# Kernel tuning notes

Hardware: AMD Instinct MI355X
Metric: run time of the kernel (lower is better)

Reference implementation:

```python
import jax, jax.numpy as jnp
import numpy as np

EMBED_DIM = 768
MAX_LEN = 1024
ALPHA = 0.99
BATCH = 16


def setup_inputs() -> dict:
    key = jax.random.key(0)
    k1, k2, k3 = jax.random.split(key, 3)
    x = jax.random.normal(k1, (BATCH, MAX_LEN, EMBED_DIM), dtype=jnp.float32)
    # torch nn.Linear(embed_dim, 3*embed_dim): store weight as [in, out] for x @ W
    scale = 1.0 / np.sqrt(EMBED_DIM)
    W_qkv = jax.random.uniform(k2, (EMBED_DIM, 3 * EMBED_DIM), dtype=jnp.float32,
                               minval=-scale, maxval=scale)
    b_qkv = jax.random.uniform(k3, (3 * EMBED_DIM,), dtype=jnp.float32,
                               minval=-scale, maxval=scale)
    return {"x": x, "W_qkv": W_qkv, "b_qkv": b_qkv}


def _retention_mask(sl, alpha, dtype):
    # M[i, j] = alpha**(i - j) if i >= j else 0 (causal tril * decay)
    i = jnp.arange(sl)[:, None]
    j = jnp.arange(sl)[None, :]
    causal = i >= j
    # compute decay only where causal to avoid huge alpha**(negative) values
    exponent = jnp.where(causal, (i - j).astype(dtype), 0.0)
    decay = jnp.asarray(alpha, dtype) ** exponent
    return jnp.where(causal, decay, jnp.zeros((), dtype))


def reference(x, W_qkv, b_qkv):
    bs, sl, d = x.shape
    qkv = x @ W_qkv + b_qkv                      # [B, S, 3D]
    q, k, v = jnp.split(qkv, 3, axis=-1)         # each [B, S, D]
    M = _retention_mask(sl, ALPHA, x.dtype)      # [S, S]
    scores = jnp.einsum('bsd,btd->bst', q, k) / jnp.sqrt(jnp.asarray(d, x.dtype))
    out = jnp.einsum('bst,btd->bsd', scores * M[None, :, :], v)
    return out
```

## Files before the change

### kernel.cpp

```cpp
#include <hip/hip_runtime.h>
#include <hip/hip_bf16.h>


#define SEQ   1024
#define DIM   768
#define ND3   2304

typedef __attribute__((ext_vector_type(8))) short bf16x8;
typedef __attribute__((ext_vector_type(4))) float f32x4;

#define L2A     (-0.014499569695115089f)
#define RSQRTD  (0.03608439182435161f)

__device__ __forceinline__ unsigned short f2bf(float x) {
  union { float f; unsigned u; } v; v.f = x;
  unsigned r = v.u + 0x7FFFu + ((v.u >> 16) & 1u);
  return (unsigned short)(r >> 16);
}

__device__ __forceinline__ void gload16(const void* g, void* l) {
  __builtin_amdgcn_global_load_lds(
      (const __attribute__((address_space(1))) void*)g,
      (__attribute__((address_space(3))) void*)l, 16, 0, 0);
}

__device__ __forceinline__ void gemm_core(
    const unsigned short* gA, const unsigned short* gA2,
    const unsigned short* gB, const unsigned short* gB2,
    char* lsA, char* lsB, int nt, int wid, int lane, f32x4 acc[2][4]) {
  int lr = lane & 15, lg = lane >> 4;
  int wm = wid >> 1, wn = wid & 1;
  int rdA = (wm * 32 + lr) * 128 + ((lg ^ (lr & 7)) << 4);
  int rdB = (wn * 64 + lr) * 128 + ((lg ^ (lr & 7)) << 4);
  int wo = wid * 2048;

#define STAGE(t, par) do {                                                    \
    int lo_ = ((par) << 14) + wo;                                             \
    gload16(gA  + (size_t)(t) * 64, lsA + lo_);                               \
    gload16(gA2 + (size_t)(t) * 64, lsA + lo_ + 1024);                        \
    gload16(gB  + (size_t)(t) * 64, lsB + lo_);                               \
    gload16(gB2 + (size_t)(t) * 64, lsB + lo_ + 1024);                        \
  } while (0)

  STAGE(0, 0);
  STAGE(1, 1);
  asm volatile("s_waitcnt vmcnt(4)" ::: "memory");
  __builtin_amdgcn_s_barrier();
  asm volatile("" ::: "memory");

  for (int t = 0; t < nt; ++t) {
    int pbase = (t & 1) << 14;
    bf16x8 aF[2][2], bF[2][4];
#pragma unroll
    for (int kh = 0; kh < 2; ++kh) {
#pragma unroll
      for (int f = 0; f < 2; ++f)
        aF[kh][f] = *(const bf16x8*)(lsA + pbase + ((rdA + f * 2048) ^ (kh << 6)));
#pragma unroll
      for (int n = 0; n < 4; ++n)
        bF[kh][n] = *(const bf16x8*)(lsB + pbase + ((rdB + n * 2048) ^ (kh << 6)));
    }
    __builtin_amdgcn_s_setprio(1);
#pragma unroll
    for (int kh = 0; kh < 2; ++kh)
#pragma unroll
      for (int f = 0; f < 2; ++f)
#pragma unroll
        for (int n = 0; n < 4; ++n)
          acc[f][n] = __builtin_amdgcn_mfma_f32_16x16x32_bf16(aF[kh][f], bF[kh][n], acc[f][n], 0, 0, 0);
    __builtin_amdgcn_s_setprio(0);

    if (t == nt - 1) break;
    __builtin_amdgcn_s_barrier();
    asm volatile("" ::: "memory");
    if (t + 2 < nt) {
      STAGE(t + 2, t & 1);
      asm volatile("s_waitcnt vmcnt(4)" ::: "memory");
    } else {
      asm volatile("s_waitcnt vmcnt(0)" ::: "memory");
    }
    __builtin_amdgcn_s_barrier();
    asm volatile("" ::: "memory");
  }
#undef STAGE
}

__global__ void convert_x(const float* __restrict__ x, unsigned short* __restrict__ xb) {
  size_t i = ((size_t)blockIdx.x * 256 + threadIdx.x) * 8;
  float4 f0 = *(const float4*)(x + i);
  float4 f1 = *(const float4*)(x + i + 4);
  bf16x8 v;
  v[0] = (short)f2bf(f0.x); v[1] = (short)f2bf(f0.y);
  v[2] = (short)f2bf(f0.z); v[3] = (short)f2bf(f0.w);
  v[4] = (short)f2bf(f1.x); v[5] = (short)f2bf(f1.y);
  v[6] = (short)f2bf(f1.z); v[7] = (short)f2bf(f1.w);
  *(bf16x8*)(xb + i) = v;
}

__global__ void transpose_w(const float* __restrict__ W, unsigned short* __restrict__ Wt) {
  __shared__ float tile[64][65];
  int n0 = (blockIdx.x % 36) * 64;
  int k0 = (blockIdx.x / 36) * 64;
  int tx = threadIdx.x & 63, ty = threadIdx.x >> 6;
#pragma unroll
  for (int p = 0; p < 16; ++p) {
    int k = ty + p * 4;
    tile[k][tx] = W[(size_t)(k0 + k) * ND3 + n0 + tx];
  }
  __syncthreads();
#pragma unroll
  for (int p = 0; p < 16; ++p) {
    int n = ty + p * 4;
    Wt[(size_t)(n0 + n) * DIM + k0 + tx] = f2bf(tile[tx][n]);
  }
}

__global__ void __launch_bounds__(512, 4) qkv_g(
    const unsigned short* __restrict__ xb, const unsigned short* __restrict__ Wt,
    const float* __restrict__ bias,
    unsigned short* __restrict__ Qs, unsigned short* __restrict__ Ks,
    unsigned short* __restrict__ Vt) {
  __shared__ char lsA[32768];
  __shared__ char lsB[32768];
  int bid = (blockIdx.x & 7) * 288 + (blockIdx.x >> 3);
  int mt = bid / 18, ntb = bid % 18;
  int m0 = mt * 128, n0 = ntb * 128;

  int tid = threadIdx.x, lane = tid & 63, wid = tid >> 6;
  int l8 = lane >> 3, cs = ((lane & 7) ^ l8) << 3;
  int srow = wid * 16 + l8;

  const unsigned short* gA = xb + (size_t)(m0 + srow) * DIM + cs;
  const unsigned short* gB = Wt + (size_t)(n0 + srow) * DIM + cs;

  f32x4 acc[2][4] = {};
  gemm_core(gA, gA + 8 * DIM, gB, gB + 8 * DIM, lsA, lsB, 12, wid, lane, acc);

  int wm = wid >> 1, wn = wid & 1;
  int lr = lane & 15, lg = lane >> 4;
  float bia[4];
#pragma unroll
  for (int n = 0; n < 4; ++n) bia[n] = bias[n0 + wn * 64 + n * 16 + lr];

  if (ntb < 6) {
#pragma unroll
    for (int f = 0; f < 2; ++f)
#pragma unroll
      for (int r = 0; r < 4; ++r) {
        int mg = m0 + wm * 32 + f * 16 + lg * 4 + r;
        int b = mg >> 10, s = mg & 1023;
        float sc = exp2f((float)s * L2A) * RSQRTD;
        unsigned short* dst = Qs + ((size_t)b * SEQ + s) * DIM + n0 + wn * 64 + lr;
#pragma unroll
        for (int n = 0; n < 4; ++n)
          dst[n * 16] = f2bf((acc[f][n][r] + bia[n]) * sc);
      }
  } else if (ntb < 12) {
#pragma unroll
    for (int f = 0; f < 2; ++f)
#pragma unroll
      for (int r = 0; r < 4; ++r) {
        int mg = m0 + wm * 32 + f * 16 + lg * 4 + r;
        int b = mg >> 10, s = mg & 1023;
        float sc = exp2f(-(float)s * L2A);
        unsigned short* dst = Ks + ((size_t)b * SEQ + s) * DIM + (n0 - DIM) + wn * 64 + lr;
#pragma unroll
        for (int n = 0; n < 4; ++n)
          dst[n * 16] = f2bf((acc[f][n][r] + bia[n]) * sc);
      }
  } else {
#pragma unroll
    for (int f = 0; f < 2; ++f)
#pragma unroll
      for (int r = 0; r < 4; ++r) {
        int mg = m0 + wm * 32 + f * 16 + lg * 4 + r;
        int b = mg >> 10, s = mg & 1023;
        int d = (n0 - 2 * DIM) + wn * 64 + lr;
        unsigned short* dst = Vt + ((size_t)b * DIM + d) * SEQ + s;
#pragma unroll
        for (int n = 0; n < 4; ++n)
          dst[(size_t)n * 16 * SEQ] = f2bf(acc[f][n][r] + bia[n]);
      }
  }
}

__global__ void __launch_bounds__(512, 4) score_g(
    const unsigned short* __restrict__ Qs, const unsigned short* __restrict__ Ks,
    unsigned short* __restrict__ Sm, int b_base) {
  __shared__ char lsA[32768];
  __shared__ char lsB[32768];
  int bid = (blockIdx.x & 7) * (gridDim.x >> 3) + (blockIdx.x >> 3);
  int t = bid % 36, bl = bid / 36;
  int b = b_base + bl;
  int it = 0;
  while (t >= it + 1) { t -= it + 1; it++; }
  int jt = t;
  int m0 = it * 128, n0 = jt * 128;
  const unsigned short* A  = Qs + (size_t)b * SEQ * DIM;
  const unsigned short* Bt = Ks + (size_t)b * SEQ * DIM;
  unsigned short* Smp = Sm + (size_t)bl * SEQ * SEQ;

  int tid = threadIdx.x, lane = tid & 63, wid = tid >> 6;
  int l8 = lane >> 3, cs = ((lane & 7) ^ l8) << 3;
  int srow = wid * 16 + l8;

  const unsigned short* gA = A  + (size_t)(m0 + srow) * DIM + cs;
  const unsigned short* gB = Bt + (size_t)(n0 + srow) * DIM + cs;

  f32x4 acc[2][4] = {};
  gemm_core(gA, gA + 8 * DIM, gB, gB + 8 * DIM, lsA, lsB, 12, wid, lane, acc);

  int wm = wid >> 1, wn = wid & 1;
  int lr = lane & 15, lg = lane >> 4;
#pragma unroll
  for (int f = 0; f < 2; ++f)
#pragma unroll
    for (int n = 0; n < 4; ++n) {
      int j = n0 + wn * 64 + n * 16 + lr;
#pragma unroll
      for (int r = 0; r < 4; ++r) {
        int i = m0 + wm * 32 + f * 16 + lg * 4 + r;
        float v = acc[f][n][r];
        if (j > i) v = 0.0f;
        Smp[(size_t)i * SEQ + j] = f2bf(v);
      }
    }
}

__global__ void __launch_bounds__(512, 4) pv_g(
    const unsigned short* __restrict__ Sm, const unsigned short* __restrict__ Vt,
    float* __restrict__ out, int b_base, int gsz) {
  __shared__ char lsA[32768];
  __shared__ char lsB[32768];
  int it = 7 - blockIdx.x / (gsz * 6);
  int rem = blockIdx.x % (gsz * 6);
  int bl = rem / 6, dt = rem % 6;
  int b = b_base + bl;
  int m0 = it * 128, n0 = dt * 128;
  const unsigned short* A  = Sm + (size_t)bl * SEQ * SEQ;
  const unsigned short* Bt = Vt + (size_t)b * DIM * SEQ;
  int nt = (it + 1) * 2;

  int tid = threadIdx.x, lane = tid & 63, wid = tid >> 6;
  int l8 = lane >> 3, cs = ((lane & 7) ^ l8) << 3;
  int srow = wid * 16 + l8;

  const unsigned short* gA = A  + (size_t)(m0 + srow) * SEQ + cs;
  const unsigned short* gB = Bt + (size_t)(n0 + srow) * SEQ + cs;

  f32x4 acc[2][4] = {};
  gemm_core(gA, gA + 8 * SEQ, gB, gB + 8 * SEQ, lsA, lsB, nt, wid, lane, acc);

  int wm = wid >> 1, wn = wid & 1;
  int lr = lane & 15, lg = lane >> 4;
#pragma unroll
  for (int f = 0; f < 2; ++f)
#pragma unroll
    for (int n = 0; n < 4; ++n) {
      int d = n0 + wn * 64 + n * 16 + lr;
#pragma unroll
      for (int r = 0; r < 4; ++r) {
        int i = m0 + wm * 32 + f * 16 + lg * 4 + r;
        out[((size_t)b * SEQ + i) * DIM + d] = acc[f][n][r];
      }
    }
}

extern "C" void kernel_launch(void* const* d_in, const int* in_sizes, int n_in,
                              void* d_out, int out_size, void* d_ws, size_t ws_size,
                              hipStream_t stream) {
  const float* x    = (const float*)d_in[0];
  const float* W    = (const float*)d_in[1];
  const float* bias = (const float*)d_in[2];
  float* out = (float*)d_out;

  char* ws = (char*)d_ws;
  unsigned short* Wt = (unsigned short*)(ws);
  unsigned short* Qs = (unsigned short*)(ws + 3538944);
  unsigned short* Ks = (unsigned short*)(ws + 3538944 + 25165824);
  unsigned short* Vt = (unsigned short*)(ws + 3538944 + 2 * 25165824);
  unsigned short* Sm = (unsigned short*)(ws + 3538944 + 3 * 25165824);
  unsigned short* xb = (unsigned short*)d_out;

  size_t smBase = 3538944 + 3 * (size_t)25165824;
  int gsz = (ws_size >= smBase + (size_t)16 * SEQ * SEQ * 2) ? 16 : 8;
  int ngrp = 16 / gsz;

  transpose_w<<<36 * 12, 256, 0, stream>>>(W, Wt);
  convert_x<<<6144, 256, 0, stream>>>(x, xb);
  qkv_g<<<2304, 512, 0, stream>>>(xb, Wt, bias, Qs, Ks, Vt);
  for (int g = 0; g < ngrp; ++g) {
    score_g<<<gsz * 36, 512, 0, stream>>>(Qs, Ks, Sm, g * gsz);
    pv_g<<<gsz * 48, 512, 0, stream>>>(Sm, Vt, out, g * gsz, gsz);
  }
}
```

Before: 149.5 us.

## Merge prep kernels, vectorize V-transpose stores, align LDS, XCD-aware pv mapping

Combines the x-conversion and W-transpose kernels into one launch, removing a kernel launch and the gap between the two. The V-transpose epilogue now writes four consecutive sequence positions as one ushort4 store instead of four scalar strided stores. LDS buffers are aligned to 1024 bytes. The pv block index is remapped so each XCD handles its own set of batches, meant to improve L2 locality for the Sm and Vt reads. The __syncthreads in the merged kernel now sits inside a branch that depends on the block index, which stays legal because the branch is uniform across each block.

```diff
diff --git a/kernel.cpp b/kernel.cpp
--- a/kernel.cpp
+++ b/kernel.cpp
@@ -85,33 +85,36 @@
 #undef STAGE
 }
 
-__global__ void convert_x(const float* __restrict__ x, unsigned short* __restrict__ xb) {
-  size_t i = ((size_t)blockIdx.x * 256 + threadIdx.x) * 8;
-  float4 f0 = *(const float4*)(x + i);
-  float4 f1 = *(const float4*)(x + i + 4);
-  bf16x8 v;
-  v[0] = (short)f2bf(f0.x); v[1] = (short)f2bf(f0.y);
-  v[2] = (short)f2bf(f0.z); v[3] = (short)f2bf(f0.w);
-  v[4] = (short)f2bf(f1.x); v[5] = (short)f2bf(f1.y);
-  v[6] = (short)f2bf(f1.z); v[7] = (short)f2bf(f1.w);
-  *(bf16x8*)(xb + i) = v;
-}
-
-__global__ void transpose_w(const float* __restrict__ W, unsigned short* __restrict__ Wt) {
+__global__ void prep(const float* __restrict__ x, unsigned short* __restrict__ xb,
+                     const float* __restrict__ W, unsigned short* __restrict__ Wt) {
   __shared__ float tile[64][65];
-  int n0 = (blockIdx.x % 36) * 64;
-  int k0 = (blockIdx.x / 36) * 64;
-  int tx = threadIdx.x & 63, ty = threadIdx.x >> 6;
-#pragma unroll
-  for (int p = 0; p < 16; ++p) {
-    int k = ty + p * 4;
-    tile[k][tx] = W[(size_t)(k0 + k) * ND3 + n0 + tx];
-  }
-  __syncthreads();
-#pragma unroll
-  for (int p = 0; p < 16; ++p) {
-    int n = ty + p * 4;
-    Wt[(size_t)(n0 + n) * DIM + k0 + tx] = f2bf(tile[tx][n]);
+  int bid = blockIdx.x;
+  if (bid < 6144) {
+    size_t i = ((size_t)bid * 256 + threadIdx.x) * 8;
+    float4 f0 = *(const float4*)(x + i);
+    float4 f1 = *(const float4*)(x + i + 4);
+    bf16x8 v;
+    v[0] = (short)f2bf(f0.x); v[1] = (short)f2bf(f0.y);
+    v[2] = (short)f2bf(f0.z); v[3] = (short)f2bf(f0.w);
+    v[4] = (short)f2bf(f1.x); v[5] = (short)f2bf(f1.y);
+    v[6] = (short)f2bf(f1.z); v[7] = (short)f2bf(f1.w);
+    *(bf16x8*)(xb + i) = v;
+  } else {
+    int tb = bid - 6144;
+    int n0 = (tb % 36) * 64;
+    int k0 = (tb / 36) * 64;
+    int tx = threadIdx.x & 63, ty = threadIdx.x >> 6;
+#pragma unroll
+    for (int p = 0; p < 16; ++p) {
+      int k = ty + p * 4;
+      tile[k][tx] = W[(size_t)(k0 + k) * ND3 + n0 + tx];
+    }
+    __syncthreads();
+#pragma unroll
+    for (int p = 0; p < 16; ++p) {
+      int n = ty + p * 4;
+      Wt[(size_t)(n0 + n) * DIM + k0 + tx] = f2bf(tile[tx][n]);
+    }
   }
 }
 
@@ -120,8 +123,8 @@
     const float* __restrict__ bias,
     unsigned short* __restrict__ Qs, unsigned short* __restrict__ Ks,
     unsigned short* __restrict__ Vt) {
-  __shared__ char lsA[32768];
-  __shared__ char lsB[32768];
+  __shared__ __align__(1024) char lsA[32768];
+  __shared__ __align__(1024) char lsB[32768];
   int bid = (blockIdx.x & 7) * 288 + (blockIdx.x >> 3);
   int mt = bid / 18, ntb = bid % 18;
   int m0 = mt * 128, n0 = ntb * 128;
@@ -170,25 +173,28 @@
       }
   } else {
 #pragma unroll
-    for (int f = 0; f < 2; ++f)
-#pragma unroll
-      for (int r = 0; r < 4; ++r) {
-        int mg = m0 + wm * 32 + f * 16 + lg * 4 + r;
-        int b = mg >> 10, s = mg & 1023;
-        int d = (n0 - 2 * DIM) + wn * 64 + lr;
-        unsigned short* dst = Vt + ((size_t)b * DIM + d) * SEQ + s;
-#pragma unroll
-        for (int n = 0; n < 4; ++n)
-          dst[(size_t)n * 16 * SEQ] = f2bf(acc[f][n][r] + bia[n]);
-      }
+    for (int f = 0; f < 2; ++f) {
+      int mg = m0 + wm * 32 + f * 16 + lg * 4;
+      int b = mg >> 10, s0 = mg & 1023;
+#pragma unroll
+      for (int n = 0; n < 4; ++n) {
+        int d = (n0 - 2 * DIM) + wn * 64 + n * 16 + lr;
+        ushort4 v;
+        v.x = f2bf(acc[f][n][0] + bia[n]);
+        v.y = f2bf(acc[f][n][1] + bia[n]);
+        v.z = f2bf(acc[f][n][2] + bia[n]);
+        v.w = f2bf(acc[f][n][3] + bia[n]);
+        *(ushort4*)(Vt + ((size_t)b * DIM + d) * SEQ + s0) = v;
+      }
+    }
   }
 }
 
 __global__ void __launch_bounds__(512, 4) score_g(
     const unsigned short* __restrict__ Qs, const unsigned short* __restrict__ Ks,
     unsigned short* __restrict__ Sm, int b_base) {
-  __shared__ char lsA[32768];
-  __shared__ char lsB[32768];
+  __shared__ __align__(1024) char lsA[32768];
+  __shared__ __align__(1024) char lsB[32768];
   int bid = (blockIdx.x & 7) * (gridDim.x >> 3) + (blockIdx.x >> 3);
   int t = bid % 36, bl = bid / 36;
   int b = b_base + bl;
@@ -230,11 +236,16 @@
 __global__ void __launch_bounds__(512, 4) pv_g(
     const unsigned short* __restrict__ Sm, const unsigned short* __restrict__ Vt,
     float* __restrict__ out, int b_base, int gsz) {
-  __shared__ char lsA[32768];
-  __shared__ char lsB[32768];
-  int it = 7 - blockIdx.x / (gsz * 6);
-  int rem = blockIdx.x % (gsz * 6);
-  int bl = rem / 6, dt = rem % 6;
+  __shared__ __align__(1024) char lsA[32768];
+  __shared__ __align__(1024) char lsB[32768];
+  int xcd = blockIdx.x & 7;
+  int j = blockIdx.x >> 3;
+  int nbx = gsz >> 3;
+  int perit = nbx * 6;
+  int it = 7 - j / perit;
+  int rem = j % perit;
+  int bl = xcd * nbx + rem / 6;
+  int dt = rem % 6;
   int b = b_base + bl;
   int m0 = it * 128, n0 = dt * 128;
   const unsigned short* A  = Sm + (size_t)bl * SEQ * SEQ;
@@ -286,8 +297,7 @@
   int gsz = (ws_size >= smBase + (size_t)16 * SEQ * SEQ * 2) ? 16 : 8;
   int ngrp = 16 / gsz;
 
-  transpose_w<<<36 * 12, 256, 0, stream>>>(W, Wt);
-  convert_x<<<6144, 256, 0, stream>>>(x, xb);
+  prep<<<6576, 256, 0, stream>>>(x, xb, W, Wt);
   qkv_g<<<2304, 512, 0, stream>>>(xb, Wt, bias, Qs, Ks, Vt);
   for (int g = 0; g < ngrp; ++g) {
     score_g<<<gsz * 36, 512, 0, stream>>>(Qs, Ks, Sm, g * gsz);
```

Measured after the change: 138.9 us (median of 2 runs). -7.1%, faster.
